# Performance work log

Measured on AMD Instinct MI355X. Metric: run time of the kernel, lower is better.

## Reference

```python
import jax, jax.numpy as jnp
import numpy as np
from jax import lax

B, C, H, W = 2, 256, 200, 336
N_ROI = 512
NUM_CLASSES = 81


def setup_inputs() -> dict:
    key = jax.random.key(0)
    ks = jax.random.split(key, 20)
    feat = jax.random.normal(ks[0], (B, C, H, W), dtype=jnp.float32)
    # proposals in feature-map coordinates, x1<x2, y1<y2
    x1 = jax.random.uniform(ks[1], (N_ROI,)) * (0.7 * W)
    y1 = jax.random.uniform(ks[2], (N_ROI,)) * (0.7 * H)
    x2 = jnp.minimum(x1 + 8.0 + jax.random.uniform(ks[3], (N_ROI,)) * (0.29 * W), W - 1.0)
    y2 = jnp.minimum(y1 + 8.0 + jax.random.uniform(ks[4], (N_ROI,)) * (0.29 * H), H - 1.0)
    boxes = jnp.stack([x1, y1, x2, y2], axis=1).astype(jnp.float32)
    batch_idx = jax.random.randint(ks[5], (N_ROI,), 0, B)
    s = 0.02
    def rn(k, shape):
        return s * jax.random.normal(k, shape, dtype=jnp.float32)
    d_in = C * 7 * 7  # 12544
    return {
        'feat': feat, 'boxes': boxes,
        'bw1': rn(ks[6], (d_in, 1024)), 'bw2': rn(ks[7], (1024, 1024)), 'bwo': rn(ks[8], (1024, 4 * NUM_CLASSES)),
        'cw1': rn(ks[9], (d_in, 1024)), 'cw2': rn(ks[10], (1024, 1024)), 'cwo': rn(ks[11], (1024, NUM_CLASSES)),
        'm1': rn(ks[12], (C, C, 3, 3)), 'm2': rn(ks[13], (C, C, 3, 3)),
        'm3': rn(ks[14], (C, C, 3, 3)), 'm4': rn(ks[15], (C, C, 3, 3)),
        'mdc': rn(ks[16], (C, C, 2, 2)),  # IOHW for conv_transpose
        'mpr': rn(ks[17], (NUM_CLASSES, C, 1, 1)),
        'batch_idx': batch_idx,
    }


def roi_align(feat, boxes, batch_idx, out_size, sampling_ratio=2):
    """Bilinear RoIAlign. feat [B,C,H,W], boxes [N,4] (x1,y1,x2,y2) in feature coords.
    Returns [N,C,out_size,out_size]."""
    N = boxes.shape[0]
    _, Cc, Hh, Ww = feat.shape
    P = out_size * sampling_ratio
    x1, y1, x2, y2 = boxes[:, 0], boxes[:, 1], boxes[:, 2], boxes[:, 3]
    steps = (jnp.arange(P, dtype=feat.dtype) + 0.5) / P  # [P]
    xs = jnp.clip(x1[:, None] + steps[None, :] * (x2 - x1)[:, None], 0.0, Ww - 1.0)  # [N,P]
    ys = jnp.clip(y1[:, None] + steps[None, :] * (y2 - y1)[:, None], 0.0, Hh - 1.0)  # [N,P]
    x0 = jnp.floor(xs).astype(jnp.int32); x1i = jnp.minimum(x0 + 1, Ww - 1); lx = xs - x0
    y0 = jnp.floor(ys).astype(jnp.int32); y1i = jnp.minimum(y0 + 1, Hh - 1); ly = ys - y0
    b = batch_idx[:, None, None]                   # [N,1,1]
    yy0, yy1 = y0[:, :, None], y1i[:, :, None]     # [N,P,1]
    xx0, xx1 = x0[:, None, :], x1i[:, None, :]     # [N,1,P]
    # gathers -> [N,P,P,C] (advanced indices first, channel slice last)
    f00 = feat[b, :, yy0, xx0]
    f01 = feat[b, :, yy0, xx1]
    f10 = feat[b, :, yy1, xx0]
    f11 = feat[b, :, yy1, xx1]
    wy = ly[:, :, None, None]  # [N,P,1,1]
    wx = lx[:, None, :, None]  # [N,1,P,1]
    val = (f00 * (1 - wy) * (1 - wx) + f01 * (1 - wy) * wx
           + f10 * wy * (1 - wx) + f11 * wy * wx)  # [N,P,P,C]
    pooled = val.reshape(N, out_size, sampling_ratio, out_size, sampling_ratio, Cc).mean(axis=(2, 4))
    return pooled.transpose(0, 3, 1, 2)  # [N,C,out,out]


def _conv(x, w, pad='SAME'):
    return lax.conv_general_dilated(x, w, (1, 1), pad,
                                    dimension_numbers=('NCHW', 'OIHW', 'NCHW'))


def reference(feat, boxes, bw1, bw2, bwo, cw1, cw2, cwo,
              m1, m2, m3, m4, mdc, mpr, batch_idx):
    # RoIAlign (post-NMS proposals) -> box / cls / mask heads
    r7 = roi_align(feat, boxes, batch_idx, 7, 2)          # [N,C,7,7]
    flat = r7.reshape(r7.shape[0], -1)                    # [N, C*49]
    box_result = jax.nn.relu(jax.nn.relu(flat @ bw1) @ bw2) @ bwo   # [N, 4*classes]
    cls_result = jax.nn.relu(jax.nn.relu(flat @ cw1) @ cw2) @ cwo   # [N, classes]
    x = roi_align(feat, boxes, batch_idx, 14, 2)          # [N,C,14,14]
    for w in (m1, m2, m3, m4):
        x = jax.nn.relu(_conv(x, w))
    x = jax.nn.relu(lax.conv_transpose(x, mdc, (2, 2), 'VALID',
                                       dimension_numbers=('NCHW', 'IOHW', 'NCHW')))  # [N,C,28,28]
    mask_result = _conv(x, mpr)                           # [N, classes, 28, 28]
    return (box_result, cls_result, mask_result)
```

## Files before the change

### kernel.cpp

```cpp
#include <hip/hip_runtime.h>
#include <stdint.h>

#define BB 2
#define CC 256
#define HH 200
#define WW 336
#define NROI 512
#define NCLS 81

typedef __attribute__((ext_vector_type(8))) short bf16x8;
typedef __attribute__((ext_vector_type(4))) float f32x4;

__device__ inline unsigned short f2bf(float f) {
  unsigned int u = __builtin_bit_cast(unsigned int, f);
  u += 0x7fffu + ((u >> 16) & 1u);
  return (unsigned short)(u >> 16);
}
__device__ inline float bf2f(unsigned short h) {
  unsigned int u = ((unsigned int)h) << 16;
  return __builtin_bit_cast(float, u);
}

__device__ inline void gl_lds(const void* gp, void* lp) {
  __builtin_amdgcn_global_load_lds(
      (const __attribute__((address_space(1))) unsigned int*)gp,
      (__attribute__((address_space(3))) unsigned int*)lp, 16, 0, 0);
}

__global__ void k_nchw2nhwc(const float* __restrict__ src, unsigned short* __restrict__ dst) {
  __shared__ float t[32][33];
  int b = blockIdx.z;
  int p0 = blockIdx.x * 32;
  int c0 = blockIdx.y * 32;
  int tx = threadIdx.x & 31, ty = threadIdx.x >> 5;
  const float* s = src + (size_t)b * CC * HH * WW;
  unsigned short* d = dst + (size_t)b * CC * HH * WW;
#pragma unroll
  for (int q = 0; q < 4; ++q)
    t[ty + q * 8][tx] = s[(size_t)(c0 + ty + q * 8) * (HH * WW) + p0 + tx];
  __syncthreads();
#pragma unroll
  for (int q = 0; q < 4; ++q)
    d[(size_t)(p0 + ty + q * 8) * CC + c0 + tx] = f2bf(t[tx][ty + q * 8]);
}

__global__ void k_repack_convw4(const float* __restrict__ w0, const float* __restrict__ w1,
                                const float* __restrict__ w2, const float* __restrict__ w3,
                                unsigned short* __restrict__ wT) {
  int d = blockIdx.x * 256 + threadIdx.x;
  if (d >= 589824) return;
  int which = blockIdx.y;
  const float* w = (which == 0) ? w0 : (which == 1) ? w1 : (which == 2) ? w2 : w3;
  int c = d & 255, o = (d >> 8) & 255, t = d >> 16;
  wT[(size_t)which * 589824 + d] = f2bf(w[o * 2304 + c * 9 + t]);
}

__global__ void k_repack_deconv(const float* __restrict__ mdc, unsigned short* __restrict__ wd) {
  int d = blockIdx.x * 256 + threadIdx.x;
  if (d >= 262144) return;
  int c = d & 255, o = (d >> 8) & 255, tap = d >> 16;
  int r = tap >> 1, s = tap & 1;
  wd[d] = f2bf(mdc[c * 1024 + o * 4 + (1 - r) * 2 + (1 - s)]);
}

__global__ void k_repack_mpr(const float* __restrict__ mpr, unsigned short* __restrict__ mT) {
  int d = blockIdx.x * 256 + threadIdx.x;
  if (d >= 32768) return;
  int c = d & 255, o = d >> 8;
  mT[d] = (o < 81) ? f2bf(mpr[o * 256 + c]) : (unsigned short)0;
}

__global__ void k_repack_w1(const float* __restrict__ src, unsigned short* __restrict__ dst) {
  __shared__ float t[32][33];
  int s = blockIdx.x;
  int c0 = blockIdx.y * 32;
  int n0 = blockIdx.z * 32;
  int tx = threadIdx.x & 31, ty = threadIdx.x >> 5;
#pragma unroll
  for (int q = 0; q < 4; ++q)
    t[ty + q * 8][tx] = src[(size_t)((c0 + ty + q * 8) * 49 + s) * 1024 + n0 + tx];
  __syncthreads();
#pragma unroll
  for (int q = 0; q < 4; ++q)
    dst[(size_t)(n0 + ty + q * 8) * 12544 + s * 256 + c0 + tx] = f2bf(t[tx][ty + q * 8]);
}

__global__ void k_transpose_w(const float* __restrict__ src, unsigned short* __restrict__ dst,
                              int K, int Nreal, int Nphys) {
  __shared__ float t[32][33];
  int k0 = blockIdx.x * 32;
  int n0 = blockIdx.y * 32;
  int tx = threadIdx.x & 31, ty = threadIdx.x >> 5;
#pragma unroll
  for (int q = 0; q < 4; ++q) {
    int n = n0 + tx;
    t[ty + q * 8][tx] = (n < Nreal) ? src[(size_t)(k0 + ty + q * 8) * Nreal + n] : 0.f;
  }
  __syncthreads();
#pragma unroll
  for (int q = 0; q < 4; ++q) {
    int n = n0 + ty + q * 8;
    if (n < Nphys) dst[(size_t)n * K + k0 + tx] = f2bf(t[tx][ty + q * 8]);
  }
}

__global__ void k_zero_border(unsigned short* __restrict__ r14p,
                              unsigned short* __restrict__ cbufA,
                              unsigned short* __restrict__ cbufB) {
  unsigned short* base = (blockIdx.y == 0) ? r14p : (blockIdx.y == 1) ? cbufA : cbufB;
  uint4 z = {0u, 0u, 0u, 0u};
#pragma unroll
  for (int q = 0; q < 8; ++q) {
    int lin = blockIdx.x * 2048 + q * 256 + threadIdx.x;
    int row = lin >> 5, u4 = lin & 31;
    int img = row / 60, b = row - img * 60;
    int y, x;
    if (b < 16) { y = 0; x = b; }
    else if (b < 32) { y = 15; x = b - 16; }
    else { int rem = b - 32; y = 1 + (rem >> 1); x = (rem & 1) * 15; }
    int slot = img * 256 + y * 16 + x;
    ((uint4*)base)[(size_t)slot * 32 + u4] = z;
  }
}

template <int OS>
__global__ void k_roialign(const unsigned short* __restrict__ featN, const float* __restrict__ boxes,
                           const int* __restrict__ bidx, unsigned short* __restrict__ out) {
  const int S = OS * OS;
  int blk = blockIdx.x;
  int n = blk / S;
  int s = blk - n * S;
  int oy = s / OS, ox = s - oy * OS;
  int c = threadIdx.x;
  float x1 = boxes[n * 4 + 0], y1 = boxes[n * 4 + 1];
  float x2 = boxes[n * 4 + 2], y2 = boxes[n * 4 + 3];
  const unsigned short* fb = featN + (size_t)bidx[n] * HH * WW * CC;
  const float P = (float)(OS * 2);
  float acc = 0.f;
#pragma unroll
  for (int sy = 0; sy < 2; ++sy)
#pragma unroll
    for (int sx = 0; sx < 2; ++sx) {
      float xs = x1 + ((float)(ox * 2 + sx) + 0.5f) / P * (x2 - x1);
      float ys = y1 + ((float)(oy * 2 + sy) + 0.5f) / P * (y2 - y1);
      xs = fminf(fmaxf(xs, 0.f), (float)(WW - 1));
      ys = fminf(fmaxf(ys, 0.f), (float)(HH - 1));
      int x0 = (int)floorf(xs);
      int y0 = (int)floorf(ys);
      int x1i = min(x0 + 1, WW - 1);
      int y1i = min(y0 + 1, HH - 1);
      float lx = xs - (float)x0, ly = ys - (float)y0;
      float f00 = bf2f(fb[((y0 * WW + x0) << 8) + c]);
      float f01 = bf2f(fb[((y0 * WW + x1i) << 8) + c]);
      float f10 = bf2f(fb[((y1i * WW + x0) << 8) + c]);
      float f11 = bf2f(fb[((y1i * WW + x1i) << 8) + c]);
      acc += f00 * (1.f - ly) * (1.f - lx) + f01 * (1.f - ly) * lx +
             f10 * ly * (1.f - lx) + f11 * ly * lx;
    }
  acc *= 0.25f;
  if (OS == 7) {
    out[(size_t)n * 12544 + s * 256 + c] = f2bf(acc);
  } else {
    int slot = n * 256 + (oy + 1) * 16 + (ox + 1);
    out[((size_t)slot << 8) + c] = f2bf(acc);
  }
}

#define TM 128
#define TN 128
#define TK 32

__global__ __launch_bounds__(256) void k_gemm_bf16(
    const unsigned short* __restrict__ A0, const unsigned short* __restrict__ Bt0, void* __restrict__ O0p,
    const unsigned short* __restrict__ A1, const unsigned short* __restrict__ Bt1, void* __restrict__ O1p,
    int K, int Nreal, int ldO, int mode, int relu, int ki, int kj) {
  const unsigned short* A = blockIdx.z ? A1 : A0;
  const unsigned short* Bt = blockIdx.z ? Bt1 : Bt0;
  void* Op = blockIdx.z ? O1p : O0p;

  __shared__ unsigned short As[TM * TK];
  __shared__ unsigned short Bs[TN * TK];

  int tid = threadIdx.x, lane = tid & 63, w = tid >> 6;
  int m0 = blockIdx.y * TM, n0 = blockIdx.x * TN;
  int lr = lane >> 2, lc = (lane & 3) * 8;

  const unsigned short* aP[2];
  const unsigned short* bP[2];
  unsigned short* asL[2];
  unsigned short* bsL[2];
#pragma unroll
  for (int s = 0; s < 2; ++s) {
    int seg = w * 2 + s;
    aP[s] = A + (size_t)(m0 + seg * 16 + lr) * K + lc;
    bP[s] = Bt + (size_t)(n0 + seg * 16 + lr) * K + lc;
    asL[s] = As + seg * 512;
    bsL[s] = Bs + seg * 512;
  }

  f32x4 acc[4][4] = {};
  int wm = (w & 1) * 64, wn = (w >> 1) * 64;
  int qa = (lane >> 4) * 8, rl = lane & 15;

  for (int k0 = 0; k0 < K; k0 += TK) {
    gl_lds(aP[0], asL[0]);
    gl_lds(aP[1], asL[1]);
    gl_lds(bP[0], bsL[0]);
    gl_lds(bP[1], bsL[1]);
    aP[0] += TK; aP[1] += TK; bP[0] += TK; bP[1] += TK;
    __syncthreads();
    bf16x8 af[4], bfr[4];
#pragma unroll
    for (int i = 0; i < 4; ++i)
      af[i] = *(const bf16x8*)&As[(wm + i * 16 + rl) * TK + qa];
#pragma unroll
    for (int j = 0; j < 4; ++j)
      bfr[j] = *(const bf16x8*)&Bs[(wn + j * 16 + rl) * TK + qa];
#pragma unroll
    for (int i = 0; i < 4; ++i)
#pragma unroll
      for (int j = 0; j < 4; ++j)
        acc[i][j] = __builtin_amdgcn_mfma_f32_16x16x32_bf16(af[i], bfr[j], acc[i][j], 0, 0, 0);
    __syncthreads();
  }

  int col = lane & 15, rquad = (lane >> 4) * 4;
#pragma unroll
  for (int i = 0; i < 4; ++i) {
#pragma unroll
    for (int j = 0; j < 4; ++j) {
      int gn = n0 + wn + j * 16 + col;
#pragma unroll
      for (int r = 0; r < 4; ++r) {
        int gm = m0 + wm + i * 16 + rquad + r;
        float v = acc[i][j][r];
        if (relu) v = fmaxf(v, 0.f);
        if (mode == 0) {
          ((unsigned short*)Op)[(size_t)gm * ldO + gn] = f2bf(v);
        } else if (mode == 1) {
          if (gn < Nreal) ((float*)Op)[(size_t)gm * ldO + gn] = v;
        } else {
          if (gn < Nreal) {
            int nimg = gm / 196;
            int s2 = gm - nimg * 196;
            int ii = s2 / 14, jj = s2 - ii * 14;
            size_t dst = (((size_t)nimg * 81 + gn) * 28 + (2 * ii + ki)) * 28 + (2 * jj + kj);
            ((float*)Op)[dst] = v;
          }
        }
      }
    }
  }
}

__global__ __launch_bounds__(256) void k_fc1(
    const unsigned short* __restrict__ A, const unsigned short* __restrict__ Bb,
    const unsigned short* __restrict__ Bc, float* __restrict__ Opart) {
  int head = blockIdx.z >> 3, slice = blockIdx.z & 7;
  const unsigned short* Bt = head ? Bc : Bb;

  __shared__ unsigned short As[TM * TK];
  __shared__ unsigned short Bs[TN * TK];

  int tid = threadIdx.x, lane = tid & 63, w = tid >> 6;
  int m0 = blockIdx.y * TM, n0 = blockIdx.x * TN;
  int lr = lane >> 2, lc = (lane & 3) * 8;
  int kbase = slice * 1568;

  const unsigned short* aP[2];
  const unsigned short* bP[2];
  unsigned short* asL[2];
  unsigned short* bsL[2];
#pragma unroll
  for (int s = 0; s < 2; ++s) {
    int seg = w * 2 + s;
    aP[s] = A + (size_t)(m0 + seg * 16 + lr) * 12544 + kbase + lc;
    bP[s] = Bt + (size_t)(n0 + seg * 16 + lr) * 12544 + kbase + lc;
    asL[s] = As + seg * 512;
    bsL[s] = Bs + seg * 512;
  }

  f32x4 acc[4][4] = {};
  int wm = (w & 1) * 64, wn = (w >> 1) * 64;
  int qa = (lane >> 4) * 8, rl = lane & 15;

  for (int k0 = 0; k0 < 1568; k0 += TK) {
    gl_lds(aP[0], asL[0]);
    gl_lds(aP[1], asL[1]);
    gl_lds(bP[0], bsL[0]);
    gl_lds(bP[1], bsL[1]);
    aP[0] += TK; aP[1] += TK; bP[0] += TK; bP[1] += TK;
    __syncthreads();
    bf16x8 af[4], bfr[4];
#pragma unroll
    for (int i = 0; i < 4; ++i)
      af[i] = *(const bf16x8*)&As[(wm + i * 16 + rl) * TK + qa];
#pragma unroll
    for (int j = 0; j < 4; ++j)
      bfr[j] = *(const bf16x8*)&Bs[(wn + j * 16 + rl) * TK + qa];
#pragma unroll
    for (int i = 0; i < 4; ++i)
#pragma unroll
      for (int j = 0; j < 4; ++j)
        acc[i][j] = __builtin_amdgcn_mfma_f32_16x16x32_bf16(af[i], bfr[j], acc[i][j], 0, 0, 0);
    __syncthreads();
  }

  float* O = Opart + (size_t)(head * 8 + slice) * 524288;
  int col = lane & 15, rquad = (lane >> 4) * 4;
#pragma unroll
  for (int i = 0; i < 4; ++i)
#pragma unroll
    for (int j = 0; j < 4; ++j) {
      int gn = n0 + wn + j * 16 + col;
#pragma unroll
      for (int r = 0; r < 4; ++r) {
        int gm = m0 + wm + i * 16 + rquad + r;
        O[(size_t)gm * 1024 + gn] = acc[i][j][r];
      }
    }
}

__global__ void k_fc1red(const float* __restrict__ part, unsigned short* __restrict__ h1b,
                         unsigned short* __restrict__ h1c) {
  int head = blockIdx.y;
  int i = blockIdx.x * 256 + threadIdx.x;
  const float* p = part + (size_t)head * 8 * 524288 + i;
  float s = 0.f;
#pragma unroll
  for (int q = 0; q < 8; ++q) s += p[(size_t)q * 524288];
  unsigned short* h = head ? h1c : h1b;
  h[i] = f2bf(fmaxf(s, 0.f));
}

template <int PADOUT>
__global__ __launch_bounds__(512, 2) void k_conv256(const unsigned short* __restrict__ act,
                                                    const unsigned short* __restrict__ wt,
                                                    unsigned short* __restrict__ out) {
  __shared__ unsigned short As[2][16384];
  __shared__ unsigned short Bs[2][16384];

  int tid = threadIdx.x, lane = tid & 63, wv = tid >> 6;
  int mt = (blockIdx.x & 7) * 49 + (blockIdx.x >> 3);
  int m0 = mt * 256;

  int r8 = tid >> 3;
  int j8 = ((tid & 7) ^ (r8 & 7)) * 8;
  int slotA[4];
  int bElem[4];
#pragma unroll
  for (int q = 0; q < 4; ++q) {
    int row = q * 64 + r8;
    int gm = m0 + row;
    int n = gm / 196;
    int rem = gm - n * 196;
    int y = rem / 14, x = rem - y * 14;
    slotA[q] = n * 256 + (y + 1) * 16 + (x + 1);
    bElem[q] = row * 256 + j8;
  }
  int ldsU = wv * 512;

  int wr = wv >> 2, wc = wv & 3;
  int rl = lane & 15, lg = lane >> 4, e = lane & 7;
  int swz0 = ((lg) ^ e) * 8;
  int swz1 = ((4 + lg) ^ e) * 8;

  f32x4 acc[8][4] = {};

#define STAGE(S, D)                                                               \
  do {                                                                            \
    int cb_ = (S) / 9;                                                            \
    int t_ = (S) - cb_ * 9;                                                       \
    int ky_ = t_ / 3, kx_ = t_ - ky_ * 3;                                         \
    int tapd_ = (ky_ - 1) * 16 + (kx_ - 1);                                       \
    int coff_ = cb_ * 64;                                                         \
    _Pragma("unroll") for (int q = 0; q < 4; ++q)                                 \
        gl_lds(act + (size_t)(slotA[q] + tapd_) * 256 + coff_ + j8,               \
               &As[D][q * 4096 + ldsU]);                                          \
    _Pragma("unroll") for (int q = 0; q < 4; ++q)                                 \
        gl_lds(wt + (size_t)t_ * 65536 + bElem[q] + coff_,                        \
               &Bs[D][q * 4096 + ldsU]);                                          \
  } while (0)

  STAGE(0, 0);
  __syncthreads();

  for (int s = 0; s < 36; ++s) {
    int cur = s & 1;
    if (s + 1 < 36) STAGE(s + 1, cur ^ 1);
    const unsigned short* Ab = As[cur];
    const unsigned short* Bb = Bs[cur];
#pragma unroll
    for (int ks = 0; ks < 2; ++ks) {
      int sw = ks ? swz1 : swz0;
      bf16x8 a[8], b[4];
#pragma unroll
      for (int fi = 0; fi < 8; ++fi)
        a[fi] = *(const bf16x8*)&Ab[(wr * 128 + fi * 16 + rl) * 64 + sw];
#pragma unroll
      for (int fj = 0; fj < 4; ++fj)
        b[fj] = *(const bf16x8*)&Bb[(wc * 64 + fj * 16 + rl) * 64 + sw];
      __builtin_amdgcn_s_setprio(1);
#pragma unroll
      for (int fi = 0; fi < 8; ++fi)
#pragma unroll
        for (int fj = 0; fj < 4; ++fj)
          acc[fi][fj] = __builtin_amdgcn_mfma_f32_16x16x32_bf16(a[fi], b[fj], acc[fi][fj], 0, 0, 0);
      __builtin_amdgcn_s_setprio(0);
    }
    __syncthreads();
  }
#undef STAGE

  int col = lane & 15, rquad = lg * 4;
#pragma unroll
  for (int fi = 0; fi < 8; ++fi) {
#pragma unroll
    for (int r = 0; r < 4; ++r) {
      int gm = m0 + wr * 128 + fi * 16 + rquad + r;
      size_t rowbase;
      if (PADOUT) {
        int n = gm / 196;
        int rem = gm - n * 196;
        int y = rem / 14, x = rem - y * 14;
        rowbase = ((size_t)(n * 256 + (y + 1) * 16 + (x + 1))) << 8;
      } else {
        rowbase = (size_t)gm << 8;
      }
#pragma unroll
      for (int fj = 0; fj < 4; ++fj) {
        int gn = wc * 64 + fj * 16 + col;
        out[rowbase + gn] = f2bf(fmaxf(acc[fi][fj][r], 0.f));
      }
    }
  }
}

extern "C" void kernel_launch(void* const* d_in, const int* in_sizes, int n_in,
                              void* d_out, int out_size, void* d_ws, size_t ws_size,
                              hipStream_t stream) {
  (void)in_sizes; (void)n_in; (void)out_size; (void)ws_size;
  const float* feat = (const float*)d_in[0];
  const float* boxes = (const float*)d_in[1];
  const float* bw1 = (const float*)d_in[2];
  const float* bw2 = (const float*)d_in[3];
  const float* bwo = (const float*)d_in[4];
  const float* cw1 = (const float*)d_in[5];
  const float* cw2 = (const float*)d_in[6];
  const float* cwo = (const float*)d_in[7];
  const float* m1 = (const float*)d_in[8];
  const float* m2 = (const float*)d_in[9];
  const float* m3 = (const float*)d_in[10];
  const float* m4 = (const float*)d_in[11];
  const float* mdc = (const float*)d_in[12];
  const float* mpr = (const float*)d_in[13];
  const int* bidx = (const int*)d_in[14];

  char* p = (char*)d_ws;
  unsigned short* featN = (unsigned short*)p; p += 68812800;
  unsigned short* cbufA = featN;
  unsigned short* cbufB = (unsigned short*)p; p += 67108864;
  float* fc1part = (float*)cbufB;
  unsigned short* r14p = (unsigned short*)p;  p += 67108864;
  unsigned short* dflat = (unsigned short*)p; p += 51380224;
  unsigned short* ddec = (unsigned short*)p;  p += 51380224;
  unsigned short* r7b = (unsigned short*)p;   p += 12845056;
  unsigned short* h1b = (unsigned short*)p;   p += 1048576;
  unsigned short* h1c = (unsigned short*)p;   p += 1048576;
  unsigned short* h2b = (unsigned short*)p;   p += 1048576;
  unsigned short* h2c = (unsigned short*)p;   p += 1048576;
  unsigned short* wTb = (unsigned short*)p;   p += 4718592;
  unsigned short* wdb = (unsigned short*)p;   p += 524288;
  unsigned short* mprTb = (unsigned short*)p; p += 65536;
  unsigned short* bw1b = (unsigned short*)p;  p += 25690112;
  unsigned short* cw1b = (unsigned short*)p;  p += 25690112;
  unsigned short* bw2b = (unsigned short*)p;  p += 2097152;
  unsigned short* cw2b = (unsigned short*)p;  p += 2097152;
  unsigned short* bwob = (unsigned short*)p;  p += 786432;
  unsigned short* cwob = (unsigned short*)p;  p += 262144;

  float* outBox = (float*)d_out;
  float* outCls = outBox + 512 * 324;
  float* outMask = outCls + 512 * 81;

  k_nchw2nhwc<<<dim3(2100, 8, 2), 256, 0, stream>>>(feat, featN);
  k_repack_convw4<<<dim3(2304, 4), 256, 0, stream>>>(m1, m2, m3, m4, wTb);
  k_repack_deconv<<<dim3(1024), 256, 0, stream>>>(mdc, wdb);
  k_repack_mpr<<<dim3(128), 256, 0, stream>>>(mpr, mprTb);
  k_repack_w1<<<dim3(49, 8, 32), 256, 0, stream>>>(bw1, bw1b);
  k_repack_w1<<<dim3(49, 8, 32), 256, 0, stream>>>(cw1, cw1b);
  k_transpose_w<<<dim3(32, 32), 256, 0, stream>>>(bw2, bw2b, 1024, 1024, 1024);
  k_transpose_w<<<dim3(32, 32), 256, 0, stream>>>(cw2, cw2b, 1024, 1024, 1024);
  k_transpose_w<<<dim3(32, 12), 256, 0, stream>>>(bwo, bwob, 1024, 324, 384);
  k_transpose_w<<<dim3(32, 4), 256, 0, stream>>>(cwo, cwob, 1024, 81, 128);

  k_roialign<7><<<dim3(512 * 49), 256, 0, stream>>>(featN, boxes, bidx, r7b);
  k_roialign<14><<<dim3(512 * 196), 256, 0, stream>>>(featN, boxes, bidx, r14p);

  k_fc1<<<dim3(8, 4, 16), 256, 0, stream>>>(r7b, bw1b, cw1b, fc1part);
  k_fc1red<<<dim3(2048, 2), 256, 0, stream>>>(fc1part, h1b, h1c);
  k_gemm_bf16<<<dim3(8, 4, 2), 256, 0, stream>>>(h1b, bw2b, h2b, h1c, cw2b, h2c,
                                                 1024, 1024, 1024, 0, 1, 0, 0);
  k_gemm_bf16<<<dim3(3, 4, 1), 256, 0, stream>>>(h2b, bwob, outBox, h2b, bwob, outBox,
                                                 1024, 324, 324, 1, 0, 0, 0);
  k_gemm_bf16<<<dim3(1, 4, 1), 256, 0, stream>>>(h2c, cwob, outCls, h2c, cwob, outCls,
                                                 1024, 81, 81, 1, 0, 0, 0);

  k_zero_border<<<dim3(480, 3), 256, 0, stream>>>(r14p, cbufA, cbufB);
  k_conv256<1><<<dim3(392), 512, 0, stream>>>(r14p, wTb + 0 * 589824, cbufA);
  k_conv256<1><<<dim3(392), 512, 0, stream>>>(cbufA, wTb + 1 * 589824, cbufB);
  k_conv256<1><<<dim3(392), 512, 0, stream>>>(cbufB, wTb + 2 * 589824, cbufA);
  k_conv256<0><<<dim3(392), 512, 0, stream>>>(cbufA, wTb + 3 * 589824, dflat);

  for (int r = 0; r < 2; ++r)
    for (int s = 0; s < 2; ++s) {
      int tap = r * 2 + s;
      k_gemm_bf16<<<dim3(2, 784, 1), 256, 0, stream>>>(
          dflat, wdb + tap * 65536, ddec, dflat, wdb, ddec,
          256, 256, 256, 0, 1, 0, 0);
      k_gemm_bf16<<<dim3(1, 784, 1), 256, 0, stream>>>(
          ddec, mprTb, outMask, ddec, mprTb, outMask,
          256, 81, 0, 2, 0, r, s);
    }
}
```

Before: 1.677 ms.

## Split conv GEMM main loop into quadrant phases with fine-grained barriers

Restructures the implicit-GEMM conv main loop so each K-stage runs as four quadrant MFMA phases, interleaving LDS fragment loads and global-to-LDS prefetch of the A and B tiles between them. The single __syncthreads is replaced by explicit vmcnt waits and several s_barriers, in the style of a ping-pong schedule. The aim is to overlap memory traffic with MFMA work and cut register pressure by loading only half the fragments at a time. The extra barriers and hand-counted vmcnt waits add sync overhead and risk ordering mistakes, for example B is staged into the next buffer while other waves may still be reading it.

```diff
diff --git a/kernel.cpp b/kernel.cpp
--- a/kernel.cpp
+++ b/kernel.cpp
@@ -362,12 +362,14 @@
 
   int wr = wv >> 2, wc = wv & 3;
   int rl = lane & 15, lg = lane >> 4, e = lane & 7;
-  int swz0 = ((lg) ^ e) * 8;
-  int swz1 = ((4 + lg) ^ e) * 8;
+  int s0 = (lg ^ e) * 8;
+  int s1 = ((4 + lg) ^ e) * 8;
+  int rowA = (wr * 128 + rl) * 64;
+  int rowB = (wc * 64 + rl) * 64;
 
   f32x4 acc[8][4] = {};
 
-#define STAGE(S, D)                                                               \
+#define STAGE_A(S, D)                                                             \
   do {                                                                            \
     int cb_ = (S) / 9;                                                            \
     int t_ = (S) - cb_ * 9;                                                       \
@@ -377,40 +379,81 @@
     _Pragma("unroll") for (int q = 0; q < 4; ++q)                                 \
         gl_lds(act + (size_t)(slotA[q] + tapd_) * 256 + coff_ + j8,               \
                &As[D][q * 4096 + ldsU]);                                          \
+  } while (0)
+
+#define STAGE_B(S, D)                                                             \
+  do {                                                                            \
+    int cb_ = (S) / 9;                                                            \
+    int t_ = (S) - cb_ * 9;                                                       \
+    int coff_ = cb_ * 64;                                                         \
     _Pragma("unroll") for (int q = 0; q < 4; ++q)                                 \
         gl_lds(wt + (size_t)t_ * 65536 + bElem[q] + coff_,                        \
                &Bs[D][q * 4096 + ldsU]);                                          \
   } while (0)
 
-  STAGE(0, 0);
-  __syncthreads();
+#define LOAD_A(QI)                                                                \
+  _Pragma("unroll") for (int fi = 0; fi < 4; ++fi) {                              \
+    a[fi][0] = *(const bf16x8*)&Ab[rowA + (QI)*4096 + fi * 1024 + s0];            \
+    a[fi][1] = *(const bf16x8*)&Ab[rowA + (QI)*4096 + fi * 1024 + s1];            \
+  }
+
+#define LOAD_B(QJ, BREG)                                                          \
+  _Pragma("unroll") for (int fj = 0; fj < 2; ++fj) {                              \
+    BREG[fj][0] = *(const bf16x8*)&Bb[rowB + (QJ)*2048 + fj * 1024 + s0];         \
+    BREG[fj][1] = *(const bf16x8*)&Bb[rowB + (QJ)*2048 + fj * 1024 + s1];         \
+  }
+
+#define QUAD(QI, QJ, BREG)                                                        \
+  __builtin_amdgcn_s_setprio(1);                                                  \
+  _Pragma("unroll") for (int fi = 0; fi < 4; ++fi)                                \
+  _Pragma("unroll") for (int fj = 0; fj < 2; ++fj) {                              \
+    acc[(QI)*4 + fi][(QJ)*2 + fj] = __builtin_amdgcn_mfma_f32_16x16x32_bf16(      \
+        a[fi][0], BREG[fj][0], acc[(QI)*4 + fi][(QJ)*2 + fj], 0, 0, 0);           \
+    acc[(QI)*4 + fi][(QJ)*2 + fj] = __builtin_amdgcn_mfma_f32_16x16x32_bf16(      \
+        a[fi][1], BREG[fj][1], acc[(QI)*4 + fi][(QJ)*2 + fj], 0, 0, 0);           \
+  }                                                                               \
+  __builtin_amdgcn_s_setprio(0);
+
+  STAGE_A(0, 0);
+  STAGE_B(0, 0);
 
   for (int s = 0; s < 36; ++s) {
-    int cur = s & 1;
-    if (s + 1 < 36) STAGE(s + 1, cur ^ 1);
+    int cur = s & 1, nxt = cur ^ 1;
     const unsigned short* Ab = As[cur];
     const unsigned short* Bb = Bs[cur];
-#pragma unroll
-    for (int ks = 0; ks < 2; ++ks) {
-      int sw = ks ? swz1 : swz0;
-      bf16x8 a[8], b[4];
-#pragma unroll
-      for (int fi = 0; fi < 8; ++fi)
-        a[fi] = *(const bf16x8*)&Ab[(wr * 128 + fi * 16 + rl) * 64 + sw];
-#pragma unroll
-      for (int fj = 0; fj < 4; ++fj)
-        b[fj] = *(const bf16x8*)&Bb[(wc * 64 + fj * 16 + rl) * 64 + sw];
-      __builtin_amdgcn_s_setprio(1);
-#pragma unroll
-      for (int fi = 0; fi < 8; ++fi)
-#pragma unroll
-        for (int fj = 0; fj < 4; ++fj)
-          acc[fi][fj] = __builtin_amdgcn_mfma_f32_16x16x32_bf16(a[fi], b[fj], acc[fi][fj], 0, 0, 0);
-      __builtin_amdgcn_s_setprio(0);
+    if (s < 35) {
+      STAGE_A(s + 1, nxt);
+      asm volatile("s_waitcnt vmcnt(4)" ::: "memory");
+    } else {
+      asm volatile("s_waitcnt vmcnt(0)" ::: "memory");
     }
-    __syncthreads();
-  }
-#undef STAGE
+    __builtin_amdgcn_s_barrier();
+    __builtin_amdgcn_sched_barrier(0);
+
+    bf16x8 a[4][2], b0[2][2], b1[2][2];
+    LOAD_A(0);
+    LOAD_B(0, b0);
+    __builtin_amdgcn_s_barrier();
+    QUAD(0, 0, b0);
+    __builtin_amdgcn_s_barrier();
+    LOAD_B(1, b1);
+    if (s < 35) STAGE_B(s + 1, nxt);
+    __builtin_amdgcn_s_barrier();
+    QUAD(0, 1, b1);
+    __builtin_amdgcn_s_barrier();
+    LOAD_A(1);
+    __builtin_amdgcn_s_barrier();
+    QUAD(1, 0, b0);
+    __builtin_amdgcn_s_barrier();
+    QUAD(1, 1, b1);
+    __builtin_amdgcn_s_barrier();
+    __builtin_amdgcn_sched_barrier(0);
+  }
+#undef STAGE_A
+#undef STAGE_B
+#undef LOAD_A
+#undef LOAD_B
+#undef QUAD
 
   int col = lane & 15, rquad = lg * 4;
 #pragma unroll
```

New measurement: 1.651 ms. About the same (-1.5%).
